# Kernel optimization log

Hardware: AMD Instinct MI355X
Metric: run time of the kernel (lower is better)

## Reference

```python
import jax, jax.numpy as jnp
import numpy as np

COLDNESS = 1.0
ITERATION = 10


def setup_inputs() -> dict:
    key = jax.random.key(0)
    k1, k2 = jax.random.split(key)
    B, N, T = 16, 8, 65536
    inp = jax.random.normal(k1, (B, N, T), dtype=jnp.float32)
    tgt = jax.random.normal(k2, (B, N, T), dtype=jnp.float32)
    return {"input": inp, "target": tgt}


def reference(input, target):
    # Pairwise MSE criterion: loss[b, i, j] = mean_t (input[b,i,t] - target[b,j,t])^2
    diff = input[:, :, None, :] - target[:, None, :, :]        # [B, N, N, T]
    possible_loss = jnp.mean(diff * diff, axis=-1)             # [B, N, N]

    # Sinkhorn-Knopp normalization in log space
    Z = -COLDNESS * possible_loss
    for _ in range(ITERATION):
        Z = Z - jax.nn.logsumexp(Z, axis=1, keepdims=True)
        Z = Z - jax.nn.logsumexp(Z, axis=2, keepdims=True)

    permutation_matrix = jnp.exp(Z)                            # [B, N, N]
    loss = jnp.sum((possible_loss + Z / COLDNESS) * permutation_matrix, axis=(1, 2))
    loss = jnp.mean(loss)                                      # batch_mean=True
    pattern = jnp.argmax(permutation_matrix, axis=2)           # [B, N]
    return loss, pattern
```

## Files before the change

kernel.cpp:

```cpp
#include <hip/hip_runtime.h>
#include <hip/hip_bf16.h>


#define BATCH 16
#define NROW 8
#define TLEN 65536
#define CHUNKS 64
#define THREADS 256

__global__ __launch_bounds__(THREADS)
void sinkpit_dist_kernel(const float* __restrict__ x,
                         const float* __restrict__ y,
                         float* __restrict__ ws) {
    const int b     = blockIdx.y;
    const int chunk = blockIdx.x;
    const int tid   = threadIdx.x;
    const int lane  = tid & 63;
    const int wave  = tid >> 6;

    const float* xb = x + (size_t)b * NROW * TLEN;
    const float* yb = y + (size_t)b * NROW * TLEN;
    const int t0 = chunk * (TLEN / CHUNKS) + tid * 4;

    float4 yv[8], xv[8];
    #pragma unroll
    for (int j = 0; j < 8; ++j)
        yv[j] = *(const float4*)(yb + (size_t)j * TLEN + t0);
    #pragma unroll
    for (int i = 0; i < 8; ++i)
        xv[i] = *(const float4*)(xb + (size_t)i * TLEN + t0);

    float a[64];
    #pragma unroll
    for (int i = 0; i < 8; ++i) {
        #pragma unroll
        for (int j = 0; j < 8; ++j) {
            float d0 = xv[i].x - yv[j].x;
            float d1 = xv[i].y - yv[j].y;
            float d2 = xv[i].z - yv[j].z;
            float d3 = xv[i].w - yv[j].w;
            a[i * 8 + j] = ((d0 * d0 + d1 * d1) + (d2 * d2 + d3 * d3));
        }
    }

    #pragma unroll
    for (int o = 32; o >= 1; o >>= 1) {
        const bool up = (lane & o) != 0;
        #pragma unroll
        for (int c = 0; c < o; ++c) {
            float send = up ? a[c] : a[c + o];
            float recv = __shfl_xor(send, o);
            float keep = up ? a[c + o] : a[c];
            a[c] = keep + recv;
        }
    }

    __shared__ float red[4][64];
    red[wave][lane] = a[0];
    __syncthreads();
    if (tid < 64) {
        float v = red[0][tid] + red[1][tid] + red[2][tid] + red[3][tid];
        atomicAdd(&ws[b * 64 + tid], v);
    }
}

__global__ __launch_bounds__(1024)
void sinkpit_sinkhorn_kernel(const float* __restrict__ ws,
                             float* __restrict__ out) {
    const int tid  = threadIdx.x;
    const int b    = tid >> 6;
    const int lane = tid & 63;
    const int i    = lane >> 3;
    const int j    = lane & 7;

    const float poison = __uint_as_float(0xAAAAAAAAu);
    const float ssum = ws[b * 64 + lane] - poison;

    const float S = ssum * (1.0f / (float)TLEN);
    float Z = -S;

    for (int it = 0; it < 10; ++it) {
        float m = Z;
        m = fmaxf(m, __shfl_xor(m, 8));
        m = fmaxf(m, __shfl_xor(m, 16));
        m = fmaxf(m, __shfl_xor(m, 32));
        float e = __expf(Z - m);
        e += __shfl_xor(e, 8);
        e += __shfl_xor(e, 16);
        e += __shfl_xor(e, 32);
        Z -= m + __logf(e);
        m = Z;
        m = fmaxf(m, __shfl_xor(m, 1));
        m = fmaxf(m, __shfl_xor(m, 2));
        m = fmaxf(m, __shfl_xor(m, 4));
        e = __expf(Z - m);
        e += __shfl_xor(e, 1);
        e += __shfl_xor(e, 2);
        e += __shfl_xor(e, 4);
        Z -= m + __logf(e);
    }

    const float P = __expf(Z);
    float contrib = (S + Z) * P;

    float tot = contrib;
    tot += __shfl_xor(tot, 32);
    tot += __shfl_xor(tot, 16);
    tot += __shfl_xor(tot, 8);
    tot += __shfl_xor(tot, 4);
    tot += __shfl_xor(tot, 2);
    tot += __shfl_xor(tot, 1);

    __shared__ float lossred[BATCH];
    if (lane == 0) lossred[b] = tot;

    float v = Z;
    int   idx = j;
    {
        float ov; int oi;
        ov = __shfl_xor(v, 1); oi = __shfl_xor(idx, 1);
        if (ov > v || (ov == v && oi < idx)) { v = ov; idx = oi; }
        ov = __shfl_xor(v, 2); oi = __shfl_xor(idx, 2);
        if (ov > v || (ov == v && oi < idx)) { v = ov; idx = oi; }
        ov = __shfl_xor(v, 4); oi = __shfl_xor(idx, 4);
        if (ov > v || (ov == v && oi < idx)) { v = ov; idx = oi; }
    }
    if (j == 0) out[1 + b * NROW + i] = (float)idx;

    __syncthreads();
    if (tid == 0) {
        float L = 0.0f;
        #pragma unroll
        for (int bb = 0; bb < BATCH; ++bb) L += lossred[bb];
        out[0] = L * (1.0f / (float)BATCH);
    }
}

extern "C" void kernel_launch(void* const* d_in, const int* in_sizes, int n_in,
                              void* d_out, int out_size, void* d_ws, size_t ws_size,
                              hipStream_t stream) {
    const float* inp = (const float*)d_in[0];
    const float* tgt = (const float*)d_in[1];
    float* out = (float*)d_out;
    float* ws  = (float*)d_ws;

    dim3 grid(CHUNKS, BATCH);
    sinkpit_dist_kernel<<<grid, THREADS, 0, stream>>>(inp, tgt, ws);
    sinkpit_sinkhorn_kernel<<<1, BATCH * 64, 0, stream>>>(ws, out);
}
```

Before: 100.4 us.

## Fuse Sinkhorn step into distance kernel via last-block atomic counters

Merges the two kernels into one launch. A per-batch atomic counter picks the last-arriving block, which then runs the Sinkhorn iterations for that batch. A second global counter picks the last batch to compute the mean loss. This removes the second kernel launch and the dependency gap between kernels, and spreads the Sinkhorn work across 16 blocks instead of one. In exchange it adds atomic traffic and relies on the workspace starting at the poison value, the same assumption the old code already made.

```diff
diff --git a/kernel.cpp b/kernel.cpp
--- a/kernel.cpp
+++ b/kernel.cpp
@@ -7,11 +7,13 @@
 #define TLEN 65536
 #define CHUNKS 64
 #define THREADS 256
+#define POISON_U 0xAAAAAAAAu
 
 __global__ __launch_bounds__(THREADS)
-void sinkpit_dist_kernel(const float* __restrict__ x,
-                         const float* __restrict__ y,
-                         float* __restrict__ ws) {
+void sinkpit_fused_kernel(const float* __restrict__ x,
+                          const float* __restrict__ y,
+                          float* __restrict__ ws,
+                          float* __restrict__ out) {
     const int b     = blockIdx.y;
     const int chunk = blockIdx.x;
     const int tid   = threadIdx.x;
@@ -58,25 +60,30 @@
     __shared__ float red[4][64];
     red[wave][lane] = a[0];
     __syncthreads();
-    if (tid < 64) {
-        float v = red[0][tid] + red[1][tid] + red[2][tid] + red[3][tid];
-        atomicAdd(&ws[b * 64 + tid], v);
+    if (wave != 0) return;
+
+    {
+        float v = red[0][lane] + red[1][lane] + red[2][lane] + red[3][lane];
+        atomicAdd(&ws[b * 64 + lane], v);
     }
-}
+    asm volatile("s_waitcnt vmcnt(0)" ::: "memory");
 
-__global__ __launch_bounds__(1024)
-void sinkpit_sinkhorn_kernel(const float* __restrict__ ws,
-                             float* __restrict__ out) {
-    const int tid  = threadIdx.x;
-    const int b    = tid >> 6;
-    const int lane = tid & 63;
-    const int i    = lane >> 3;
-    const int j    = lane & 7;
+    int last = 0;
+    if (lane == 0) {
+        unsigned old = atomicAdd((unsigned*)(ws + BATCH * 64 + b), 1u);
+        last = (old == POISON_U + (unsigned)(CHUNKS - 1)) ? 1 : 0;
+    }
+    last = __shfl(last, 0);
+    if (!last) return;
 
-    const float poison = __uint_as_float(0xAAAAAAAAu);
-    const float ssum = ws[b * 64 + lane] - poison;
+    const int i = lane >> 3;
+    const int j = lane & 7;
+    const float poison = __uint_as_float(POISON_U);
 
-    const float S = ssum * (1.0f / (float)TLEN);
+    float s = __hip_atomic_load(&ws[b * 64 + lane],
+                                __ATOMIC_RELAXED, __HIP_MEMORY_SCOPE_AGENT);
+    s -= poison;
+    const float S = s * (1.0f / (float)TLEN);
     float Z = -S;
 
     for (int it = 0; it < 10; ++it) {
@@ -101,9 +108,8 @@
     }
 
     const float P = __expf(Z);
-    float contrib = (S + Z) * P;
+    float tot = (S + Z) * P;
 
-    float tot = contrib;
     tot += __shfl_xor(tot, 32);
     tot += __shfl_xor(tot, 16);
     tot += __shfl_xor(tot, 8);
@@ -111,12 +117,11 @@
     tot += __shfl_xor(tot, 2);
     tot += __shfl_xor(tot, 1);
 
-    __shared__ float lossred[BATCH];
-    if (lane == 0) lossred[b] = tot;
+    if (lane == 0) atomicExch(&ws[BATCH * 64 + BATCH + b], tot);
 
-    float v = Z;
-    int   idx = j;
     {
+        float v = Z;
+        int   idx = j;
         float ov; int oi;
         ov = __shfl_xor(v, 1); oi = __shfl_xor(idx, 1);
         if (ov > v || (ov == v && oi < idx)) { v = ov; idx = oi; }
@@ -124,14 +129,25 @@
         if (ov > v || (ov == v && oi < idx)) { v = ov; idx = oi; }
         ov = __shfl_xor(v, 4); oi = __shfl_xor(idx, 4);
         if (ov > v || (ov == v && oi < idx)) { v = ov; idx = oi; }
+        if (j == 0) out[1 + b * NROW + i] = (float)idx;
     }
-    if (j == 0) out[1 + b * NROW + i] = (float)idx;
 
-    __syncthreads();
-    if (tid == 0) {
+    asm volatile("s_waitcnt vmcnt(0)" ::: "memory");
+
+    int lastg = 0;
+    if (lane == 0) {
+        unsigned oldg = atomicAdd((unsigned*)(ws + BATCH * 64 + 2 * BATCH), 1u);
+        lastg = (oldg == POISON_U + (unsigned)(BATCH - 1)) ? 1 : 0;
+    }
+    lastg = __shfl(lastg, 0);
+    if (!lastg) return;
+
+    if (lane == 0) {
         float L = 0.0f;
         #pragma unroll
-        for (int bb = 0; bb < BATCH; ++bb) L += lossred[bb];
+        for (int bb = 0; bb < BATCH; ++bb)
+            L += __hip_atomic_load(&ws[BATCH * 64 + BATCH + bb],
+                                   __ATOMIC_RELAXED, __HIP_MEMORY_SCOPE_AGENT);
         out[0] = L * (1.0f / (float)BATCH);
     }
 }
@@ -145,6 +161,5 @@
     float* ws  = (float*)d_ws;
 
     dim3 grid(CHUNKS, BATCH);
-    sinkpit_dist_kernel<<<grid, THREADS, 0, stream>>>(inp, tgt, ws);
-    sinkpit_sinkhorn_kernel<<<1, BATCH * 64, 0, stream>>>(ws, out);
+    sinkpit_fused_kernel<<<grid, THREADS, 0, stream>>>(inp, tgt, ws, out);
 }
```

Result: slower. 106.9 us (+6.5%).
